# Kernel optimization log

Measured on AMD Instinct MI355X. Metric: run time of the kernel, lower is better.

The kernel has to match this reference:

```python
import jax, jax.numpy as jnp
import numpy as np

ROUTINGS = 3
NUM_CAPSULE = 32
DIM_CAPSULE = 64
K_EPSILON = 1e-7  # keras K.epsilon()


def squash(x, axis=-1):
    s = jnp.sum(jnp.square(x), axis=axis, keepdims=True) + K_EPSILON
    scale = jnp.sqrt(s) / (0.5 + s)
    return scale * x


def setup_inputs() -> dict:
    key = jax.random.key(0)
    k1, k2 = jax.random.split(key)
    B, N_in, D_in = 32, 1024, 512
    u = jax.random.normal(k1, (B, N_in, D_in), dtype=jnp.float32)
    # glorot_uniform for capsule_kernel (conv1d width-1 kernel == dense matrix)
    fan_out = NUM_CAPSULE * DIM_CAPSULE
    limit = float(np.sqrt(6.0 / (D_in + fan_out)))
    W = jax.random.uniform(k2, (D_in, fan_out), jnp.float32, -limit, limit)
    return {"u": u, "W": W}


def reference(u, W):
    B, N_in, _ = u.shape
    # K.conv1d with width-1 kernel == matmul, then reshape
    u_hat = (u @ W).reshape(B, N_in, NUM_CAPSULE, DIM_CAPSULE)
    u_hat = jnp.transpose(u_hat, (0, 2, 1, 3))  # [B, N_out, N_in, D]
    b = jnp.zeros(u_hat.shape[:3], u_hat.dtype)  # [B, N_out, N_in]
    vj = None
    for i in range(ROUTINGS):
        Wv = jax.nn.softmax(b, axis=1)  # softmax over output capsules (axis=1)
        vj = jnp.einsum('bon,bond->bod', Wv, u_hat)  # batch_dot(Wv,u_hat,[2,2])
        if i < ROUTINGS - 1:
            # K.l2_normalize(vj) with default axis=None -> global L2 norm
            norm = jnp.sqrt(jnp.maximum(jnp.sum(jnp.square(vj)), 1e-12))
            vjn = vj / norm
            b = jnp.einsum('bod,bond->bon', vjn, u_hat)  # batch_dot(vj,u_hat,[2,3])
    return squash(vj)
```

## Files before the change

kernel.cpp:

```cpp
#include <hip/hip_runtime.h>
#include <hip/hip_bf16.h>


constexpr int B = 32, N = 1024, K = 512, O = 32, D = 64, F = 2048;
constexpr int NT = 32;
constexpr int ST = 72;
constexpr int STT = 36;

typedef __attribute__((ext_vector_type(8))) short bf16x8;
typedef __attribute__((ext_vector_type(4))) float f32x4;

__device__ inline unsigned int pk_hi(float x, float y) {
  union { __hip_bfloat162 h; unsigned int u; } c;
  c.h = __float22bfloat162_rn(float2{x, y});
  return c.u;
}
__device__ inline unsigned short bf16_1(float x) {
  return (unsigned short)(pk_hi(x, 0.f) & 0xffffu);
}
__device__ inline void split2(float x, unsigned short& h, unsigned short& l) {
  h = bf16_1(x);
  l = bf16_1(x - __uint_as_float((unsigned int)h << 16));
}
__device__ inline float bf2f(unsigned short h) {
  return __uint_as_float((unsigned int)h << 16);
}
__device__ inline int swz(int r) { return ((r >> 3) & 7) << 3; }

__device__ inline bf16x8 frag_row(const unsigned short* p, int r, int k0) {
  return *(const bf16x8*)&p[r * ST + (k0 ^ swz(r))];
}

__global__ __launch_bounds__(256) void k_prep(const float* __restrict__ u,
                                              float* __restrict__ cs_part,
                                              unsigned short* __restrict__ u_bf) {
  __shared__ float4 red[128];
  int b = blockIdx.x, ntile = blockIdx.y, n0 = ntile * 32;
  int tid = threadIdx.x;
  int kq = (tid & 127) * 4, ng = tid >> 7;
  const float* ub = u + ((size_t)b * N + n0 + ng * 16) * K + kq;
  unsigned short* ubf = u_bf + ((size_t)b * N + n0 + ng * 16) * K + kq;
  float4 a = {0.f, 0.f, 0.f, 0.f};
#pragma unroll
  for (int nn = 0; nn < 16; nn++) {
    float4 v = *(const float4*)&ub[(size_t)nn * K];
    a.x += v.x; a.y += v.y; a.z += v.z; a.w += v.w;
    uint2 p;
    p.x = pk_hi(v.x, v.y);
    p.y = pk_hi(v.z, v.w);
    *(uint2*)&ubf[(size_t)nn * K] = p;
  }
  if (ng) red[tid & 127] = a;
  __syncthreads();
  if (!ng) {
    float4 o = red[tid];
    float* cs = cs_part + ((size_t)b * 32 + ntile) * K + kq;
    cs[0] = (a.x + o.x) * (1.f / 32.f);
    cs[1] = (a.y + o.y) * (1.f / 32.f);
    cs[2] = (a.z + o.z) * (1.f / 32.f);
    cs[3] = (a.w + o.w) * (1.f / 32.f);
  }
}

__global__ __launch_bounds__(512) void k_vjt(const unsigned short* __restrict__ Sp,
                                             const float* __restrict__ cs_part,
                                             const float* __restrict__ W,
                                             float* __restrict__ ssq_part, int slot,
                                             unsigned short* __restrict__ t_hi,
                                             unsigned short* __restrict__ t_lo) {
  __shared__ __align__(16) float s_s[K];
  __shared__ float red[7][D];
  __shared__ __align__(16) float vs[D];
  int bo = blockIdx.x, b = bo >> 5, o = bo & 31;
  int d = threadIdx.x & 63, ks = threadIdx.x >> 6;
  {
    int i = threadIdx.x;
    float a = 0.f;
    if (slot == 0) {
      const float* base = cs_part + (size_t)b * 32 * K;
#pragma unroll
      for (int nt = 0; nt < 32; nt++) a += base[(size_t)nt * K + i];
    } else {
      const unsigned short* base = Sp + ((size_t)b * NT * O + o) * K;
#pragma unroll
      for (int nt = 0; nt < NT; nt++) a += bf2f(base[(size_t)nt * O * K + i]);
    }
    s_s[i] = a;
  }
  __syncthreads();
  float acc = 0.f;
  const float* Wc = W + (size_t)o * D + d;
  for (int k = ks * 64; k < ks * 64 + 64; k += 4) {
    acc += s_s[k] * Wc[(size_t)k * F] + s_s[k + 1] * Wc[(size_t)(k + 1) * F] +
           s_s[k + 2] * Wc[(size_t)(k + 2) * F] + s_s[k + 3] * Wc[(size_t)(k + 3) * F];
  }
  if (ks) red[ks - 1][d] = acc;
  __syncthreads();
  if (ks == 0) {
#pragma unroll
    for (int j = 0; j < 7; j++) acc += red[j][d];
    vs[d] = acc;
    float ss = acc * acc;
#pragma unroll
    for (int m = 32; m >= 1; m >>= 1) ss += __shfl_xor(ss, m, 64);
    if (d == 0) ssq_part[slot * 1024 + bo] = ss;
  }
  __syncthreads();
  {
    int wave = threadIdx.x >> 6, lane = threadIdx.x & 63;
    int rr = lane >> 3, dc = lane & 7;
    float4 va = *(const float4*)&vs[dc * 8];
    float4 vb = *(const float4*)&vs[dc * 8 + 4];
#pragma unroll
    for (int i = 0; i < 8; i++) {
      int kk = wave * 64 + i * 8 + rr;
      const float* Wr = W + (size_t)kk * F + o * 64 + dc * 8;
      float4 wa = *(const float4*)Wr;
      float4 wb = *(const float4*)(Wr + 4);
      float p = wa.x * va.x + wa.y * va.y + wa.z * va.z + wa.w * va.w +
                wb.x * vb.x + wb.y * vb.y + wb.z * vb.z + wb.w * vb.w;
      p += __shfl_xor(p, 1, 64);
      p += __shfl_xor(p, 2, 64);
      p += __shfl_xor(p, 4, 64);
      if (dc == 0) {
        unsigned short h, l;
        split2(p, h, l);
        t_hi[(size_t)bo * K + kk] = h;
        t_lo[(size_t)bo * K + kk] = l;
      }
    }
  }
}

__global__ __launch_bounds__(512) void k_out(const unsigned short* __restrict__ Sp,
                                             const float* __restrict__ W,
                                             float* __restrict__ out) {
  __shared__ __align__(16) float s_s[K];
  __shared__ float red[7][D];
  int bo = blockIdx.x, b = bo >> 5, o = bo & 31;
  int d = threadIdx.x & 63, ks = threadIdx.x >> 6;
  {
    const unsigned short* base = Sp + ((size_t)b * NT * O + o) * K;
    int i = threadIdx.x;
    float a = 0.f;
#pragma unroll
    for (int nt = 0; nt < NT; nt++) a += bf2f(base[(size_t)nt * O * K + i]);
    s_s[i] = a;
  }
  __syncthreads();
  float acc = 0.f;
  const float* Wc = W + (size_t)o * D + d;
  for (int k = ks * 64; k < ks * 64 + 64; k += 4) {
    acc += s_s[k] * Wc[(size_t)k * F] + s_s[k + 1] * Wc[(size_t)(k + 1) * F] +
           s_s[k + 2] * Wc[(size_t)(k + 2) * F] + s_s[k + 3] * Wc[(size_t)(k + 3) * F];
  }
  if (ks) red[ks - 1][d] = acc;
  __syncthreads();
  if (ks == 0) {
#pragma unroll
    for (int j = 0; j < 7; j++) acc += red[j][d];
    float ss = acc * acc;
#pragma unroll
    for (int m = 32; m >= 1; m >>= 1) ss += __shfl_xor(ss, m, 64);
    float s = ss + 1e-7f;
    out[(size_t)bo * D + d] = (sqrtf(s) / (0.5f + s)) * acc;
  }
}

__global__ __launch_bounds__(256, 4) void k_route(const unsigned short* __restrict__ t_hi_g,
                                                  const unsigned short* __restrict__ t_lo_g,
                                                  const unsigned short* __restrict__ u_bf,
                                                  const float* __restrict__ ssq_part,
                                                  int slot,
                                                  unsigned short* __restrict__ Sp) {
  __shared__ __align__(16) unsigned short u_hi[32 * ST];
  __shared__ unsigned short t_hi[32 * ST], t_lo[32 * ST];
  __shared__ float wv[32 * 36];
  __shared__ float psum[8 * 36];
  __shared__ float mbuf[36];
  unsigned short* wvh = t_hi;
  unsigned short* wvl = t_lo;

  const int b = blockIdx.x, n0 = blockIdx.y * 32;
  const int tid = threadIdx.x, lane = tid & 63, wave = tid >> 6;
  const int m = lane & 15, oct = lane >> 4;
  const unsigned short* ubf = u_bf + ((size_t)b * N + n0) * K;
  const unsigned short* thg = t_hi_g + (size_t)b * O * K;
  const unsigned short* tlg = t_lo_g + (size_t)b * O * K;

  const int sr = tid >> 3, sc8 = (tid & 7) * 8;
  const int scs = sc8 ^ swz(sr);

  const int mo = wave & 1, nt = wave >> 1;
  f32x4 accb = {0.f, 0.f, 0.f, 0.f};
  for (int kc = 0; kc < K; kc += 64) {
    __syncthreads();
    {
      const size_t go = (size_t)sr * K + kc + sc8;
      *(uint4*)&t_hi[sr * ST + scs] = *(const uint4*)&thg[go];
      *(uint4*)&t_lo[sr * ST + scs] = *(const uint4*)&tlg[go];
      *(uint4*)&u_hi[sr * ST + scs] = *(const uint4*)&ubf[go];
    }
    __syncthreads();
#pragma unroll
    for (int ks = 0; ks < 64; ks += 32) {
      bf16x8 ah = frag_row(t_hi, mo * 16 + m, ks + oct * 8);
      bf16x8 al = frag_row(t_lo, mo * 16 + m, ks + oct * 8);
      bf16x8 bh = frag_row(u_hi, nt * 16 + m, ks + oct * 8);
      accb = __builtin_amdgcn_mfma_f32_16x16x32_bf16(ah, bh, accb, 0, 0, 0);
      accb = __builtin_amdgcn_mfma_f32_16x16x32_bf16(al, bh, accb, 0, 0, 0);
    }
  }
  __syncthreads();
  {
    const float* sp = ssq_part + slot * 1024;
    float sa = 0.f;
#pragma unroll
    for (int j = 0; j < 4; j++) sa += sp[tid + j * 256];
    psum[tid & 255] = sa;
    __syncthreads();
    if (tid < 64) {
      float s = psum[tid] + psum[tid + 64] + psum[tid + 128] + psum[tid + 192];
#pragma unroll
      for (int mm = 32; mm >= 1; mm >>= 1) s += __shfl_xor(s, mm, 64);
      if (tid == 0) mbuf[0] = rsqrtf(fmaxf(s, 1e-12f));
    }
    __syncthreads();
  }
  const float nrm_inv = mbuf[0];
  __syncthreads();
#pragma unroll
  for (int r = 0; r < 4; r++)
    wv[(mo * 16 + oct * 4 + r) * 36 + nt * 16 + m] = accb[r] * nrm_inv;
  __syncthreads();

  {
    int n = tid & 31, g = tid >> 5;
    float m4 = -1e30f;
#pragma unroll
    for (int j = 0; j < 4; j++) m4 = fmaxf(m4, wv[(g * 4 + j) * 36 + n]);
    psum[g * 36 + n] = m4;
    __syncthreads();
    if (tid < 32) {
      float mx = psum[tid];
#pragma unroll
      for (int gg = 1; gg < 8; gg++) mx = fmaxf(mx, psum[gg * 36 + tid]);
      mbuf[tid] = mx;
    }
    __syncthreads();
    float mx = mbuf[n];
    float s4 = 0.f;
#pragma unroll
    for (int j = 0; j < 4; j++) {
      float e = __expf(wv[(g * 4 + j) * 36 + n] - mx);
      wv[(g * 4 + j) * 36 + n] = e;
      s4 += e;
    }
    psum[g * 36 + n] = s4;
    __syncthreads();
    if (tid < 32) {
      float s = 0.f;
#pragma unroll
      for (int gg = 0; gg < 8; gg++) s += psum[gg * 36 + tid];
      mbuf[tid] = 1.f / s;
    }
    __syncthreads();
    float inv = mbuf[n];
#pragma unroll
    for (int j = 0; j < 4; j++) {
      unsigned short h, l;
      split2(wv[(g * 4 + j) * 36 + n] * inv, h, l);
      wvh[(g * 4 + j) * ST + n] = h;
      wvl[(g * 4 + j) * ST + n] = l;
    }
  }
  __syncthreads();

  const int mo2 = wave & 1, kp = wave >> 1;
  const int o0 = mo2 * 16;
  bf16x8 a_h = *(const bf16x8*)&wvh[(o0 + m) * ST + oct * 8];
  bf16x8 a_l = *(const bf16x8*)&wvl[(o0 + m) * ST + oct * 8];
  unsigned short* Sb = Sp + ((size_t)b * NT + blockIdx.y) * O * K;
  for (int kc = 0; kc < K; kc += 64) {
    __syncthreads();
    {
      union { uint4 q; unsigned short s[8]; } v;
      v.q = *(const uint4*)&ubf[(size_t)sr * K + kc + sc8];
#pragma unroll
      for (int j = 0; j < 8; j++) u_hi[(sc8 + j) * STT + sr] = v.s[j];
    }
    __syncthreads();
#pragma unroll
    for (int kt = kp * 2; kt < kp * 2 + 2; kt++) {
      int c = kt * 16 + m;
      union { bf16x8 v; uint2 q[2]; } uu;
      uu.q[0] = *(const uint2*)&u_hi[c * STT + oct * 8];
      uu.q[1] = *(const uint2*)&u_hi[c * STT + oct * 8 + 4];
      f32x4 acs = {0.f, 0.f, 0.f, 0.f};
      acs = __builtin_amdgcn_mfma_f32_16x16x32_bf16(a_h, uu.v, acs, 0, 0, 0);
      acs = __builtin_amdgcn_mfma_f32_16x16x32_bf16(a_l, uu.v, acs, 0, 0, 0);
#pragma unroll
      for (int r = 0; r < 4; r++)
        Sb[(size_t)(o0 + oct * 4 + r) * K + kc + c] = bf16_1(acs[r]);
    }
  }
}

extern "C" void kernel_launch(void* const* d_in, const int* in_sizes, int n_in,
                              void* d_out, int out_size, void* d_ws, size_t ws_size,
                              hipStream_t stream) {
  const float* u = (const float*)d_in[0];
  const float* W = (const float*)d_in[1];
  float* out = (float*)d_out;

  char* ws = (char*)d_ws;
  unsigned short* Sp = (unsigned short*)ws;
  unsigned short* u_bf = Sp + (size_t)B * NT * O * K;
  unsigned short* t_hi = u_bf + (size_t)B * N * K;
  unsigned short* t_lo = t_hi + (size_t)B * O * K;
  float* cs_part = (float*)(t_lo + (size_t)B * O * K);
  float* ssq_part = cs_part + (size_t)B * 32 * K;

  k_prep<<<dim3(B, 32), 256, 0, stream>>>(u, cs_part, u_bf);
  k_vjt<<<B * O, 512, 0, stream>>>(Sp, cs_part, W, ssq_part, 0, t_hi, t_lo);
  k_route<<<dim3(B, NT), 256, 0, stream>>>(t_hi, t_lo, u_bf, ssq_part, 0, Sp);
  k_vjt<<<B * O, 512, 0, stream>>>(Sp, cs_part, W, ssq_part, 1, t_hi, t_lo);
  k_route<<<dim3(B, NT), 256, 0, stream>>>(t_hi, t_lo, u_bf, ssq_part, 1, Sp);
  k_out<<<B * O, 512, 0, stream>>>(Sp, W, out);
}
```

Baseline: 183.7 us.

## Reorder Sp partials to [b][o][nt][k] and vectorize reductions in vjt/out kernels

Changes the layout of the per-tile partial sums Sp so that all NT partials for one (b,o) pair are contiguous. k_vjt and k_out can then read them with 8-byte vector loads split across four thread groups. The s·W matvec switches from strided per-d scalar loads to coalesced float4 row loads, reduced with wave shuffles and a small shared buffer. The cost is extra shared memory and syncs, and k_route's bf16 stores now use a larger stride.

```diff
diff --git a/kernel.cpp b/kernel.cpp
--- a/kernel.cpp
+++ b/kernel.cpp
@@ -69,36 +69,75 @@
                                              unsigned short* __restrict__ t_hi,
                                              unsigned short* __restrict__ t_lo) {
   __shared__ __align__(16) float s_s[K];
-  __shared__ float red[7][D];
+  __shared__ __align__(16) float redA[3][K];
+  __shared__ __align__(16) float red2[8][D];
   __shared__ __align__(16) float vs[D];
   int bo = blockIdx.x, b = bo >> 5, o = bo & 31;
-  int d = threadIdx.x & 63, ks = threadIdx.x >> 6;
-  {
-    int i = threadIdx.x;
-    float a = 0.f;
+  int tid = threadIdx.x, w = tid >> 6, lane = tid & 63;
+  {
+    int kq = (tid & 127) * 4, ng = tid >> 7;
+    float4 a = {0.f, 0.f, 0.f, 0.f};
     if (slot == 0) {
-      const float* base = cs_part + (size_t)b * 32 * K;
-#pragma unroll
-      for (int nt = 0; nt < 32; nt++) a += base[(size_t)nt * K + i];
+      const float* base = cs_part + (size_t)b * 32 * K + kq;
+#pragma unroll
+      for (int nt = ng * 8; nt < ng * 8 + 8; nt++) {
+        float4 v = *(const float4*)&base[(size_t)nt * K];
+        a.x += v.x; a.y += v.y; a.z += v.z; a.w += v.w;
+      }
     } else {
-      const unsigned short* base = Sp + ((size_t)b * NT * O + o) * K;
-#pragma unroll
-      for (int nt = 0; nt < NT; nt++) a += bf2f(base[(size_t)nt * O * K + i]);
-    }
-    s_s[i] = a;
-  }
-  __syncthreads();
-  float acc = 0.f;
-  const float* Wc = W + (size_t)o * D + d;
-  for (int k = ks * 64; k < ks * 64 + 64; k += 4) {
-    acc += s_s[k] * Wc[(size_t)k * F] + s_s[k + 1] * Wc[(size_t)(k + 1) * F] +
-           s_s[k + 2] * Wc[(size_t)(k + 2) * F] + s_s[k + 3] * Wc[(size_t)(k + 3) * F];
-  }
-  if (ks) red[ks - 1][d] = acc;
-  __syncthreads();
-  if (ks == 0) {
-#pragma unroll
-    for (int j = 0; j < 7; j++) acc += red[j][d];
+      const unsigned short* base = Sp + ((size_t)(b * O + o)) * NT * K + kq;
+#pragma unroll
+      for (int nt = ng * 8; nt < ng * 8 + 8; nt++) {
+        uint2 v = *(const uint2*)&base[(size_t)nt * K];
+        a.x += bf2f((unsigned short)(v.x & 0xffffu));
+        a.y += bf2f((unsigned short)(v.x >> 16));
+        a.z += bf2f((unsigned short)(v.y & 0xffffu));
+        a.w += bf2f((unsigned short)(v.y >> 16));
+      }
+    }
+    if (ng) *(float4*)&redA[ng - 1][kq] = a;
+    __syncthreads();
+    if (!ng) {
+#pragma unroll
+      for (int g = 0; g < 3; g++) {
+        float4 v = *(const float4*)&redA[g][kq];
+        a.x += v.x; a.y += v.y; a.z += v.z; a.w += v.w;
+      }
+      *(float4*)&s_s[kq] = a;
+    }
+    __syncthreads();
+  }
+  {
+    int rr = lane >> 3, dc = lane & 7;
+    float4 va = {0.f, 0.f, 0.f, 0.f}, vb = {0.f, 0.f, 0.f, 0.f};
+#pragma unroll
+    for (int i = 0; i < 8; i++) {
+      int k = w * 64 + i * 8 + rr;
+      const float* Wr = W + (size_t)k * F + o * 64 + dc * 8;
+      float4 wa = *(const float4*)Wr;
+      float4 wb = *(const float4*)(Wr + 4);
+      float s = s_s[k];
+      va.x += s * wa.x; va.y += s * wa.y; va.z += s * wa.z; va.w += s * wa.w;
+      vb.x += s * wb.x; vb.y += s * wb.y; vb.z += s * wb.z; vb.w += s * wb.w;
+    }
+#pragma unroll
+    for (int mm = 8; mm <= 32; mm <<= 1) {
+      va.x += __shfl_xor(va.x, mm, 64); va.y += __shfl_xor(va.y, mm, 64);
+      va.z += __shfl_xor(va.z, mm, 64); va.w += __shfl_xor(va.w, mm, 64);
+      vb.x += __shfl_xor(vb.x, mm, 64); vb.y += __shfl_xor(vb.y, mm, 64);
+      vb.z += __shfl_xor(vb.z, mm, 64); vb.w += __shfl_xor(vb.w, mm, 64);
+    }
+    if (rr == 0) {
+      *(float4*)&red2[w][dc * 8] = va;
+      *(float4*)&red2[w][dc * 8 + 4] = vb;
+    }
+    __syncthreads();
+  }
+  if (w == 0) {
+    int d = lane;
+    float acc = 0.f;
+#pragma unroll
+    for (int g = 0; g < 8; g++) acc += red2[g][d];
     vs[d] = acc;
     float ss = acc * acc;
 #pragma unroll
@@ -107,13 +146,12 @@
   }
   __syncthreads();
   {
-    int wave = threadIdx.x >> 6, lane = threadIdx.x & 63;
     int rr = lane >> 3, dc = lane & 7;
     float4 va = *(const float4*)&vs[dc * 8];
     float4 vb = *(const float4*)&vs[dc * 8 + 4];
 #pragma unroll
     for (int i = 0; i < 8; i++) {
-      int kk = wave * 64 + i * 8 + rr;
+      int kk = w * 64 + i * 8 + rr;
       const float* Wr = W + (size_t)kk * F + o * 64 + dc * 8;
       float4 wa = *(const float4*)Wr;
       float4 wb = *(const float4*)(Wr + 4);
@@ -136,29 +174,65 @@
                                              const float* __restrict__ W,
                                              float* __restrict__ out) {
   __shared__ __align__(16) float s_s[K];
-  __shared__ float red[7][D];
+  __shared__ __align__(16) float redA[3][K];
+  __shared__ __align__(16) float red2[8][D];
   int bo = blockIdx.x, b = bo >> 5, o = bo & 31;
-  int d = threadIdx.x & 63, ks = threadIdx.x >> 6;
-  {
-    const unsigned short* base = Sp + ((size_t)b * NT * O + o) * K;
-    int i = threadIdx.x;
-    float a = 0.f;
-#pragma unroll
-    for (int nt = 0; nt < NT; nt++) a += bf2f(base[(size_t)nt * O * K + i]);
-    s_s[i] = a;
-  }
-  __syncthreads();
-  float acc = 0.f;
-  const float* Wc = W + (size_t)o * D + d;
-  for (int k = ks * 64; k < ks * 64 + 64; k += 4) {
-    acc += s_s[k] * Wc[(size_t)k * F] + s_s[k + 1] * Wc[(size_t)(k + 1) * F] +
-           s_s[k + 2] * Wc[(size_t)(k + 2) * F] + s_s[k + 3] * Wc[(size_t)(k + 3) * F];
-  }
-  if (ks) red[ks - 1][d] = acc;
-  __syncthreads();
-  if (ks == 0) {
-#pragma unroll
-    for (int j = 0; j < 7; j++) acc += red[j][d];
+  int tid = threadIdx.x, w = tid >> 6, lane = tid & 63;
+  {
+    int kq = (tid & 127) * 4, ng = tid >> 7;
+    float4 a = {0.f, 0.f, 0.f, 0.f};
+    const unsigned short* base = Sp + ((size_t)(b * O + o)) * NT * K + kq;
+#pragma unroll
+    for (int nt = ng * 8; nt < ng * 8 + 8; nt++) {
+      uint2 v = *(const uint2*)&base[(size_t)nt * K];
+      a.x += bf2f((unsigned short)(v.x & 0xffffu));
+      a.y += bf2f((unsigned short)(v.x >> 16));
+      a.z += bf2f((unsigned short)(v.y & 0xffffu));
+      a.w += bf2f((unsigned short)(v.y >> 16));
+    }
+    if (ng) *(float4*)&redA[ng - 1][kq] = a;
+    __syncthreads();
+    if (!ng) {
+#pragma unroll
+      for (int g = 0; g < 3; g++) {
+        float4 v = *(const float4*)&redA[g][kq];
+        a.x += v.x; a.y += v.y; a.z += v.z; a.w += v.w;
+      }
+      *(float4*)&s_s[kq] = a;
+    }
+    __syncthreads();
+  }
+  {
+    int rr = lane >> 3, dc = lane & 7;
+    float4 va = {0.f, 0.f, 0.f, 0.f}, vb = {0.f, 0.f, 0.f, 0.f};
+#pragma unroll
+    for (int i = 0; i < 8; i++) {
+      int k = w * 64 + i * 8 + rr;
+      const float* Wr = W + (size_t)k * F + o * 64 + dc * 8;
+      float4 wa = *(const float4*)Wr;
+      float4 wb = *(const float4*)(Wr + 4);
+      float s = s_s[k];
+      va.x += s * wa.x; va.y += s * wa.y; va.z += s * wa.z; va.w += s * wa.w;
+      vb.x += s * wb.x; vb.y += s * wb.y; vb.z += s * wb.z; vb.w += s * wb.w;
+    }
+#pragma unroll
+    for (int mm = 8; mm <= 32; mm <<= 1) {
+      va.x += __shfl_xor(va.x, mm, 64); va.y += __shfl_xor(va.y, mm, 64);
+      va.z += __shfl_xor(va.z, mm, 64); va.w += __shfl_xor(va.w, mm, 64);
+      vb.x += __shfl_xor(vb.x, mm, 64); vb.y += __shfl_xor(vb.y, mm, 64);
+      vb.z += __shfl_xor(vb.z, mm, 64); vb.w += __shfl_xor(vb.w, mm, 64);
+    }
+    if (rr == 0) {
+      *(float4*)&red2[w][dc * 8] = va;
+      *(float4*)&red2[w][dc * 8 + 4] = vb;
+    }
+    __syncthreads();
+  }
+  if (w == 0) {
+    int d = lane;
+    float acc = 0.f;
+#pragma unroll
+    for (int g = 0; g < 8; g++) acc += red2[g][d];
     float ss = acc * acc;
 #pragma unroll
     for (int m = 32; m >= 1; m >>= 1) ss += __shfl_xor(ss, m, 64);
@@ -280,7 +354,7 @@
   const int o0 = mo2 * 16;
   bf16x8 a_h = *(const bf16x8*)&wvh[(o0 + m) * ST + oct * 8];
   bf16x8 a_l = *(const bf16x8*)&wvl[(o0 + m) * ST + oct * 8];
-  unsigned short* Sb = Sp + ((size_t)b * NT + blockIdx.y) * O * K;
+  unsigned short* Sb = Sp + ((size_t)b * O * NT + blockIdx.y) * K;
   for (int kc = 0; kc < K; kc += 64) {
     __syncthreads();
     {
@@ -301,7 +375,7 @@
       acs = __builtin_amdgcn_mfma_f32_16x16x32_bf16(a_l, uu.v, acs, 0, 0, 0);
 #pragma unroll
       for (int r = 0; r < 4; r++)
-        Sb[(size_t)(o0 + oct * 4 + r) * K + kc + c] = bf16_1(acs[r]);
+        Sb[(size_t)(o0 + oct * 4 + r) * NT * K + kc + c] = bf16_1(acs[r]);
     }
   }
 }
```

New measurement: 187.9 us. +2.3%, slower.
